# Optimization experiments

Measured on AMD Instinct MI355X. Metric: run time of the kernel, lower is better.

The kernel has to match this reference:

```python
import jax, jax.numpy as jnp
import numpy as np

N_NODES = 50000
N_EDGES = 600000
IN_F = 128
HID = 128
OUT = 128
CLS = 128
N_GRAPHS = 64
LN_EPS = 1e-5


def _ln(h, g, b):
    m = jnp.mean(h, axis=-1, keepdims=True)
    v = jnp.var(h, axis=-1, keepdims=True)
    return (h - m) * jax.lax.rsqrt(v + LN_EPS) * g + b


def _segment_softmax(logits, seg, num_segments):
    m = jax.ops.segment_max(logits, seg, num_segments=num_segments)
    e = jnp.exp(logits - m[seg])
    s = jax.ops.segment_sum(e, seg, num_segments=num_segments)
    return e / s[seg]


def _gat_conv(x, src, dst, aux, w_lin, b_lin, aw1, ab1, lng, lnb, aw2, ab2):
    xl = x @ w_lin + b_lin                      # [N, out]
    sf = xl[src]                                # [E, out]
    df = xl[dst]                                # [E, out]
    ef = jnp.concatenate([sf, df, aux], axis=-1)  # [E, 2*out+2]
    h = jax.nn.relu(_ln(ef @ aw1 + ab1, lng, lnb))
    logits = h @ aw2 + ab2                      # [E, 1]
    att = _segment_softmax(logits, dst, xl.shape[0])
    num = jax.ops.segment_sum(sf * att, dst, num_segments=xl.shape[0])
    cnt = jax.ops.segment_sum(jnp.ones((src.shape[0], 1), xl.dtype), dst, num_segments=xl.shape[0])
    out = num / jnp.maximum(cnt, 1.0)           # scatter_mean (empty rows -> 0)
    return out + xl


def setup_inputs() -> dict:
    key = jax.random.key(0)
    ks = jax.random.split(key, 24)
    s = 0.05
    d = {
        'x': jax.random.normal(ks[0], (N_NODES, IN_F), jnp.float32),
        'edge_index': jax.random.randint(ks[1], (2, N_EDGES), 0, N_NODES, jnp.int64),
        'aux_info': jax.random.normal(ks[2], (N_EDGES, 2), jnp.float32),
        'batch': jnp.sort(jax.random.randint(ks[3], (N_NODES,), 0, N_GRAPHS, jnp.int64)),
        # conv1 params (in->hid)
        'w_lin1': jax.random.normal(ks[4], (IN_F, HID), jnp.float32) * s,
        'b_lin1': jnp.zeros((HID,), jnp.float32),
        'aw1_1': jax.random.normal(ks[5], (2 * HID + 2, HID), jnp.float32) * s,
        'ab1_1': jnp.zeros((HID,), jnp.float32),
        'lng1': jnp.ones((HID,), jnp.float32),
        'lnb1': jnp.zeros((HID,), jnp.float32),
        'aw2_1': jax.random.normal(ks[6], (HID, 1), jnp.float32) * s,
        'ab2_1': jnp.zeros((1,), jnp.float32),
        # conv2 params (hid->out)
        'w_lin2': jax.random.normal(ks[7], (HID, OUT), jnp.float32) * s,
        'b_lin2': jnp.zeros((OUT,), jnp.float32),
        'aw1_2': jax.random.normal(ks[8], (2 * OUT + 2, HID), jnp.float32) * s,
        'ab1_2': jnp.zeros((HID,), jnp.float32),
        'lng2': jnp.ones((HID,), jnp.float32),
        'lnb2': jnp.zeros((HID,), jnp.float32),
        'aw2_2': jax.random.normal(ks[9], (HID, 1), jnp.float32) * s,
        'ab2_2': jnp.zeros((1,), jnp.float32),
        # head
        'cls_w': jax.random.normal(ks[10], (OUT, CLS), jnp.float32) * s,
        'cls_b': jnp.zeros((CLS,), jnp.float32),
        'norm_g': jnp.ones((OUT,), jnp.float32),
        'norm_b': jnp.zeros((OUT,), jnp.float32),
    }
    return d


def reference(x, edge_index, aux_info, batch,
              w_lin1, b_lin1, aw1_1, ab1_1, lng1, lnb1, aw2_1, ab2_1,
              w_lin2, b_lin2, aw1_2, ab1_2, lng2, lnb2, aw2_2, ab2_2,
              cls_w, cls_b, norm_g, norm_b):
    src, dst = edge_index[0], edge_index[1]
    h = _gat_conv(x, src, dst, aux_info, w_lin1, b_lin1, aw1_1, ab1_1, lng1, lnb1, aw2_1, ab2_1)
    h = jax.nn.relu(h)
    h = _gat_conv(h, src, dst, aux_info, w_lin2, b_lin2, aw1_2, ab1_2, lng2, lnb2, aw2_2, ab2_2)
    h = _ln(h, norm_g, norm_b)                  # [N, out]
    fusion = jax.ops.segment_max(h, batch, num_segments=N_GRAPHS)  # global max pool
    cls = fusion @ cls_w + cls_b                # [G, cls]
    return (h, cls)
```

## Files before the change

### kernel.cpp

```cpp
#include <hip/hip_runtime.h>
#include <math.h>

typedef __attribute__((ext_vector_type(8))) short short8v;
typedef __attribute__((ext_vector_type(4))) float f32x4;
typedef __attribute__((ext_vector_type(2))) float f32x2;

__device__ __forceinline__ unsigned short f2bf(float f) {
    union { float f; unsigned int u; } v; v.f = f;
    unsigned int r = v.u + 0x7FFFu + ((v.u >> 16) & 1u);
    return (unsigned short)(r >> 16);
}
__device__ __forceinline__ float bflo(unsigned int v) {
    union { unsigned int u; float f; } x; x.u = v << 16; return x.f;
}
__device__ __forceinline__ float bfhi(unsigned int v) {
    union { unsigned int u; float f; } x; x.u = v & 0xFFFF0000u; return x.f;
}
__device__ __forceinline__ unsigned char f2fp8(float f) {
    return (unsigned char)(__builtin_amdgcn_cvt_pk_fp8_f32(f, f, 0, false) & 0xFF);
}
__device__ __forceinline__ unsigned pkrtz(float a, float b) {
    unsigned d;
    asm("v_cvt_pkrtz_f16_f32 %0, %1, %2" : "=v"(d) : "v"(a), "v"(b));
    return d;
}
__device__ __forceinline__ float fdot2a(unsigned a, unsigned b, float c) {
    float d;
    asm("v_dot2_f32_f16 %0, %1, %2, %3" : "=v"(d) : "v"(a), "v"(b), "v"(c));
    return d;
}
__device__ __forceinline__ unsigned pk_fma_f16(unsigned a, unsigned b, unsigned c) {
    unsigned d;
    asm("v_pk_fma_f16 %0, %1, %2, %3" : "=v"(d) : "v"(a), "v"(b), "v"(c));
    return d;
}
__device__ __forceinline__ unsigned pk_max0_f16(unsigned a, unsigned z) {
    unsigned d;
    asm("v_pk_max_f16 %0, %1, %2" : "=v"(d) : "v"(a), "v"(z));
    return d;
}

__global__ __launch_bounds__(256) void prep_kernel(const float* __restrict__ s0,
                                                   const float* __restrict__ s1,
                                                   const float* __restrict__ s2,
                                                   const float* __restrict__ s3,
                                                   const float* __restrict__ s4,
                                                   const float* __restrict__ s5,
                                                   unsigned short* __restrict__ Wp,
                                                   const int* __restrict__ dst,
                                                   int* __restrict__ deg, int E) {
    int b = blockIdx.x;
    if (b < 384) {
        int which = b >> 6;
        const float* W = (which == 0) ? s0 : (which == 1) ? s1 : (which == 2) ? s2
                       : (which == 3) ? s3 : (which == 4) ? s4 : s5;
        int t = (b & 63) * 256 + threadIdx.x;
        int j = t & 7, l = (t >> 3) & 63, ct = (t >> 9) & 7, ks = t >> 12;
        int k = ks * 32 + (l >> 4) * 8 + j;
        int n = ct * 16 + (l & 15);
        Wp[which * 16384 + t] = f2bf(W[k * 128 + n]);
    } else {
        int e = (b - 384) * 256 + threadIdx.x;
        if (e < E) atomicAdd(&deg[dst[e]], 1);
    }
}

__global__ __launch_bounds__(256) void scan1_kernel(const int* __restrict__ deg,
                                                    int* __restrict__ rp,
                                                    int* __restrict__ bsum, int N) {
    const int lane = threadIdx.x & 63, wid = threadIdx.x >> 6;
    int i = blockIdx.x * 256 + threadIdx.x;
    int v = (i < N) ? deg[i] : 0;
    int val = v;
#pragma unroll
    for (int off = 1; off < 64; off <<= 1) {
        int t = __shfl_up(val, off, 64);
        if (lane >= off) val += t;
    }
    __shared__ int ws[4];
    if (lane == 63) ws[wid] = val;
    __syncthreads();
    int pre = 0;
#pragma unroll
    for (int w = 0; w < 4; ++w) pre += (w < wid) ? ws[w] : 0;
    int incl = pre + val;
    if (i < N) rp[i] = incl - v;
    if (threadIdx.x == 255) bsum[blockIdx.x] = incl;
}

__global__ __launch_bounds__(256) void scan23_kernel(int* __restrict__ rp,
                                                     const int* __restrict__ bsum,
                                                     const int* __restrict__ batch,
                                                     int* __restrict__ gstart,
                                                     int* __restrict__ gend,
                                                     int N, int E) {
    const int lane = threadIdx.x & 63, wid = threadIdx.x >> 6;
    const int b = blockIdx.x;
    int v = ((int)threadIdx.x < b) ? bsum[threadIdx.x] : 0;
#pragma unroll
    for (int m = 32; m >= 1; m >>= 1) v += __shfl_xor(v, m, 64);
    __shared__ int ws[4];
    if (lane == 0) ws[wid] = v;
    __syncthreads();
    int offset = ws[0] + ws[1] + ws[2] + ws[3];
    int i = b * 256 + threadIdx.x;
    if (i < N) {
        rp[i] += offset;
        int bb = batch[i];
        if (i == 0 || batch[i - 1] != bb) gstart[bb] = i;
        if (i == N - 1 || batch[i + 1] != bb) gend[bb] = i + 1;
    }
    if (b == 0 && threadIdx.x == 0) rp[N] = E;
}

__global__ void scatter_kernel(const int* __restrict__ src, const int* __restrict__ dst,
                               const float* __restrict__ aux,
                               const int* __restrict__ rowptr, int* __restrict__ cursor,
                               uint2* __restrict__ er, int E) {
    int e = blockIdx.x * 256 + threadIdx.x;
    if (e < E) {
        int d = dst[e];
        int pos = rowptr[d] + atomicAdd(&cursor[d], 1);
        float2 a = *(const float2*)(aux + 2 * e);
        uint2 r;
        r.x = (unsigned)src[e] | ((unsigned)d << 16);
        r.y = (unsigned)f2bf(a.x) | ((unsigned)f2bf(a.y) << 16);
        er[pos] = r;
    }
}

template <int ABF>
__global__ __launch_bounds__(256) void linpq_kernel(const void* __restrict__ Av,
                                                    const unsigned short* __restrict__ WpL,
                                                    const float* __restrict__ bias,
                                                    const unsigned short* __restrict__ WpP,
                                                    const unsigned short* __restrict__ WpQ,
                                                    const float* __restrict__ ab1,
                                                    unsigned short* __restrict__ Dbf,
                                                    unsigned char* __restrict__ Vf8,
                                                    unsigned char* __restrict__ Pf8,
                                                    unsigned char* __restrict__ Qf8, int M) {
    __shared__ unsigned short lds[32][136];
    __shared__ unsigned char ldsV[32][128];
    __shared__ unsigned char ldsP[32][128];
    __shared__ unsigned char ldsQ[32][128];
    const int l = threadIdx.x & 63, w = threadIdx.x >> 6;
    const int tile = w >> 1, ch = w & 1;
    const int rowb = blockIdx.x * 32;
    const int rowbase = rowb + tile * 16;
    const int r = rowbase + (l & 15);
    const int kc = (l >> 4) * 8;

    short8v afr[4];
    if (r < M) {
        if (ABF) {
            const unsigned short* ap = (const unsigned short*)Av + (size_t)r * 128 + kc;
#pragma unroll
            for (int ks = 0; ks < 4; ++ks)
                afr[ks] = *(const short8v*)(ap + ks * 32);
        } else {
            const float* ap = (const float*)Av + (size_t)r * 128 + kc;
#pragma unroll
            for (int ks = 0; ks < 4; ++ks) {
                float4 x0 = *(const float4*)(ap + ks * 32);
                float4 x1 = *(const float4*)(ap + ks * 32 + 4);
                unsigned short u[8] = {f2bf(x0.x), f2bf(x0.y), f2bf(x0.z), f2bf(x0.w),
                                       f2bf(x1.x), f2bf(x1.y), f2bf(x1.z), f2bf(x1.w)};
                afr[ks] = *(short8v*)u;
            }
        }
    } else {
#pragma unroll
        for (int ks = 0; ks < 4; ++ks)
#pragma unroll
            for (int j = 0; j < 8; ++j) afr[ks][j] = 0;
    }

    f32x4 acc[4];
#pragma unroll
    for (int c = 0; c < 4; ++c)
#pragma unroll
        for (int j = 0; j < 4; ++j) acc[c][j] = 0.f;

    const short8v* wl = (const short8v*)WpL;
#pragma unroll
    for (int ks = 0; ks < 4; ++ks)
#pragma unroll
        for (int c = 0; c < 4; ++c)
            acc[c] = __builtin_amdgcn_mfma_f32_16x16x32_bf16(
                afr[ks], wl[(ks * 8 + ch * 4 + c) * 64 + l], acc[c], 0, 0, 0);

    const int lrb = tile * 16 + (l >> 4) * 4;
#pragma unroll
    for (int c = 0; c < 4; ++c) {
        int col = (ch * 4 + c) * 16 + (l & 15);
        float bv = bias ? bias[col] : 0.f;
#pragma unroll
        for (int j = 0; j < 4; ++j) {
            float v = acc[c][j] + bv;
            lds[lrb + j][col] = f2bf(v);
            ldsV[lrb + j][col] = f2fp8(v);
        }
    }
    __syncthreads();

    {
        int r2 = threadIdx.x >> 3, q2 = threadIdx.x & 7;
        if (rowb + r2 < M) {
            *(uint4*)(Dbf + (size_t)(rowb + r2) * 128 + q2 * 16) =
                *(uint4*)&lds[r2][q2 * 16];
            *(uint4*)(Dbf + (size_t)(rowb + r2) * 128 + q2 * 16 + 8) =
                *(uint4*)&lds[r2][q2 * 16 + 8];
            *(uint4*)(Vf8 + (size_t)(rowb + r2) * 128 + q2 * 16) =
                *(uint4*)&ldsV[r2][q2 * 16];
        }
    }

    short8v xfr[4];
#pragma unroll
    for (int ks = 0; ks < 4; ++ks)
        xfr[ks] = *(const short8v*)&lds[tile * 16 + (l & 15)][kc + ks * 32];

    f32x4 accP[4], accQ[4];
#pragma unroll
    for (int c = 0; c < 4; ++c)
#pragma unroll
        for (int j = 0; j < 4; ++j) { accP[c][j] = 0.f; accQ[c][j] = 0.f; }

    const short8v* wp = (const short8v*)WpP;
    const short8v* wq = (const short8v*)WpQ;
#pragma unroll
    for (int ks = 0; ks < 4; ++ks)
#pragma unroll
        for (int c = 0; c < 4; ++c) {
            accP[c] = __builtin_amdgcn_mfma_f32_16x16x32_bf16(
                xfr[ks], wp[(ks * 8 + ch * 4 + c) * 64 + l], accP[c], 0, 0, 0);
            accQ[c] = __builtin_amdgcn_mfma_f32_16x16x32_bf16(
                xfr[ks], wq[(ks * 8 + ch * 4 + c) * 64 + l], accQ[c], 0, 0, 0);
        }

#pragma unroll
    for (int c = 0; c < 4; ++c) {
        int col = (ch * 4 + c) * 16 + (l & 15);
        float b1v = ab1[col];
#pragma unroll
        for (int j = 0; j < 4; ++j) {
            ldsP[lrb + j][col] = f2fp8(accP[c][j]);
            ldsQ[lrb + j][col] = f2fp8(accQ[c][j] + b1v);
        }
    }
    __syncthreads();
    {
        int r2 = threadIdx.x >> 3, q2 = threadIdx.x & 7;
        if (rowb + r2 < M) {
            *(uint4*)(Pf8 + (size_t)(rowb + r2) * 128 + q2 * 16) =
                *(uint4*)&ldsP[r2][q2 * 16];
            *(uint4*)(Qf8 + (size_t)(rowb + r2) * 128 + q2 * 16) =
                *(uint4*)&ldsQ[r2][q2 * 16];
        }
    }
}

__global__ __launch_bounds__(256, 4) void attn_edge_kernel(
    const unsigned char* __restrict__ Pf8, const unsigned char* __restrict__ Qf8,
    const uint2* __restrict__ er,
    const float* __restrict__ wa0, const float* __restrict__ wa1,
    const float* __restrict__ lng, const float* __restrict__ lnb,
    const float* __restrict__ aw2, const float* __restrict__ ab2,
    float* __restrict__ wt, int E) {
    __shared__ float lwf[256];
    __shared__ unsigned lwh[192];
    {
        int idx = threadIdx.x;
        int arr = idx >> 7, rem = idx & 127;
        int par = rem >> 6, c = (rem >> 2) & 15, e = rem & 3;
        const float* sp = arr ? wa1 : wa0;
        lwf[(((arr * 16 + c) << 1) + par) * 4 + e] = sp[rem];
        if (idx < 192) {
            int a2 = idx >> 6, rem2 = idx & 63;
            int p2 = rem2 >> 5;
            int c2 = (rem2 >> 1) & 15;
            int pr = rem2 & 1;
            int chn = p2 * 64 + c2 * 4 + pr * 2;
            const float* s2 = (a2 == 0) ? lng : (a2 == 1) ? lnb : aw2;
            lwh[(((a2 * 16 + c2) << 1) + p2) * 2 + pr] = pkrtz(s2[chn], s2[chn + 1]);
        }
    }
    __syncthreads();
    const int slot = blockIdx.x * 128 + ((int)threadIdx.x >> 1);
    if (slot >= E) return;
    const int par = threadIdx.x & 1;
    const unsigned one2 = 0x3C003C00u;
    const unsigned zero2 = 0u;
    const int co = par << 6;

    uint2 ev = er[slot];
    const int sn = (int)(ev.x & 0xFFFFu);
    const int dn = (int)(ev.x >> 16);
    const float ax = bflo(ev.y), ay = bfhi(ev.y);

    const uint4* prow = (const uint4*)(Pf8 + (size_t)sn * 128 + co);
    const uint4* qrow = (const uint4*)(Qf8 + (size_t)dn * 128 + co);

    float r1 = 0.f, r2 = 0.f;
    unsigned tp[32];

#pragma unroll
    for (int g = 0; g < 4; ++g) {
        uint4 pv = prow[g];
        uint4 qv = qrow[g];
        unsigned pwa[4] = {pv.x, pv.y, pv.z, pv.w};
        unsigned qwa[4] = {qv.x, qv.y, qv.z, qv.w};
#pragma unroll
        for (int cc = 0; cc < 4; ++cc) {
            const int c = g * 4 + cc;
            f32x2 plo = __builtin_amdgcn_cvt_pk_f32_fp8((int)pwa[cc], false);
            f32x2 phi = __builtin_amdgcn_cvt_pk_f32_fp8((int)pwa[cc], true);
            f32x2 qlo = __builtin_amdgcn_cvt_pk_f32_fp8((int)qwa[cc], false);
            f32x2 qhi = __builtin_amdgcn_cvt_pk_f32_fp8((int)qwa[cc], true);
            float4 w0v = *(const float4*)&lwf[((c << 1) + par) * 4];
            float4 w1v = *(const float4*)&lwf[(((16 + c) << 1) + par) * 4];
            float t0 = plo[0] + qlo[0] + ax * w0v.x + ay * w1v.x;
            float t1 = plo[1] + qlo[1] + ax * w0v.y + ay * w1v.y;
            float t2 = phi[0] + qhi[0] + ax * w0v.z + ay * w1v.z;
            float t3 = phi[1] + qhi[1] + ax * w0v.w + ay * w1v.w;
            unsigned p0 = pkrtz(t0, t1);
            unsigned p1 = pkrtz(t2, t3);
            tp[2 * c] = p0;
            tp[2 * c + 1] = p1;
            r1 = fdot2a(p0, one2, r1);
            r1 = fdot2a(p1, one2, r1);
            r2 = fdot2a(p0, p0, r2);
            r2 = fdot2a(p1, p1, r2);
        }
    }
    r1 += __shfl_xor(r1, 1, 64);
    r2 += __shfl_xor(r2, 1, 64);
    float mean = r1 * (1.f / 128.f);
    float rstd = rsqrtf(r2 * (1.f / 128.f) - mean * mean + 1e-5f);
    float mr = mean * rstd;
    unsigned rstd2 = pkrtz(rstd, rstd);
    unsigned nmr2 = pkrtz(-mr, -mr);

    float dot = 0.f;
#pragma unroll
    for (int c = 0; c < 16; ++c) {
        unsigned base = (unsigned)(((c << 1) + par) * 2);
        uint2 gg = *(const uint2*)&lwh[base];
        uint2 ll = *(const uint2*)&lwh[64 + base];
        uint2 ww = *(const uint2*)&lwh[128 + base];
        unsigned u0 = pk_fma_f16(tp[2 * c], rstd2, nmr2);
        u0 = pk_fma_f16(u0, gg.x, ll.x);
        u0 = pk_max0_f16(u0, zero2);
        dot = fdot2a(u0, ww.x, dot);
        unsigned u1 = pk_fma_f16(tp[2 * c + 1], rstd2, nmr2);
        u1 = pk_fma_f16(u1, gg.y, ll.y);
        u1 = pk_max0_f16(u1, zero2);
        dot = fdot2a(u1, ww.y, dot);
    }
    dot += __shfl_xor(dot, 1, 64);
    if (par == 0) wt[slot] = __expf(dot + ab2[0]);
}

template <int MODE>
__global__ __launch_bounds__(256) void aggr_kernel(
    const unsigned short* __restrict__ xlbf, const unsigned char* __restrict__ Vf8,
    const float* __restrict__ wt,
    const uint2* __restrict__ er, const int* __restrict__ rowptr,
    const float* __restrict__ g, const float* __restrict__ b,
    void* __restrict__ out, int N) {
    const int lane8 = threadIdx.x & 7;
    const int v = blockIdx.x * 32 + ((int)threadIdx.x >> 3);
    if (v >= N) return;
    const int jb = lane8 * 16;

    const int s0 = rowptr[v], s1e = rowptr[v + 1];
    const int deg = s1e - s0;
    float acc[16];
#pragma unroll
    for (int k = 0; k < 16; ++k) acc[k] = 0.f;
    float wsum = 0.f;

    uint4 v0 = make_uint4(0, 0, 0, 0), v1 = v0;
    float wb0 = 0.f, wb1 = 0.f;
#define GATH2(idx, VV, WW)                                                       \
    if ((idx) < s1e) {                                                           \
        int sn_ = (int)(er[idx].x & 0xFFFFu);                                    \
        VV = *(const uint4*)(Vf8 + (size_t)sn_ * 128 + jb);                      \
        WW = wt[idx];                                                            \
    }
    GATH2(s0, v0, wb0)
    GATH2(s0 + 1, v1, wb1)

    for (int i = s0; i < s1e; i += 2) {
        uint4 c0 = v0, c1 = v1;
        float u0 = wb0;
        float u1 = (i + 1 < s1e) ? wb1 : 0.f;
        GATH2(i + 2, v0, wb0)
        GATH2(i + 3, v1, wb1)
        wsum += u0 + u1;
        unsigned d0[4] = {c0.x, c0.y, c0.z, c0.w};
        unsigned d1[4] = {c1.x, c1.y, c1.z, c1.w};
#pragma unroll
        for (int k = 0; k < 4; ++k) {
            f32x2 alo = __builtin_amdgcn_cvt_pk_f32_fp8((int)d0[k], false);
            f32x2 ahi = __builtin_amdgcn_cvt_pk_f32_fp8((int)d0[k], true);
            f32x2 blo = __builtin_amdgcn_cvt_pk_f32_fp8((int)d1[k], false);
            f32x2 bhi = __builtin_amdgcn_cvt_pk_f32_fp8((int)d1[k], true);
            acc[4 * k + 0] += u0 * alo[0] + u1 * blo[0];
            acc[4 * k + 1] += u0 * alo[1] + u1 * blo[1];
            acc[4 * k + 2] += u0 * ahi[0] + u1 * bhi[0];
            acc[4 * k + 3] += u0 * ahi[1] + u1 * bhi[1];
        }
    }
#undef GATH2

    const float ns = (deg > 0) ? 1.f / (wsum * (float)deg) : 0.f;
    float o[16];
    const unsigned short* xp = xlbf + (size_t)v * 128 + jb;
    uint4 xa = *(const uint4*)xp;
    uint4 xb = *(const uint4*)(xp + 8);
    unsigned xw[8] = {xa.x, xa.y, xa.z, xa.w, xb.x, xb.y, xb.z, xb.w};
#pragma unroll
    for (int k = 0; k < 8; ++k) {
        o[2 * k] = bflo(xw[k]) + acc[2 * k] * ns;
        o[2 * k + 1] = bfhi(xw[k]) + acc[2 * k + 1] * ns;
    }

    if (MODE == 0) {
        unsigned short* op = (unsigned short*)out + (size_t)v * 128 + jb;
        unsigned opk[8];
#pragma unroll
        for (int k = 0; k < 8; ++k)
            opk[k] = (unsigned)f2bf(fmaxf(o[2 * k], 0.f)) |
                     ((unsigned)f2bf(fmaxf(o[2 * k + 1], 0.f)) << 16);
        *(uint4*)op = make_uint4(opk[0], opk[1], opk[2], opk[3]);
        *(uint4*)(op + 8) = make_uint4(opk[4], opk[5], opk[6], opk[7]);
    } else {
        float r1 = 0.f, r2 = 0.f;
#pragma unroll
        for (int k = 0; k < 16; ++k) { r1 += o[k]; r2 = fmaf(o[k], o[k], r2); }
#pragma unroll
        for (int mk = 4; mk >= 1; mk >>= 1) {
            r1 += __shfl_xor(r1, mk, 64);
            r2 += __shfl_xor(r2, mk, 64);
        }
        float mean = r1 * (1.f / 128.f);
        float rstd = rsqrtf(r2 * (1.f / 128.f) - mean * mean + 1e-5f);
        float mr = mean * rstd;
        float* op = (float*)out + (size_t)v * 128 + jb;
#pragma unroll
        for (int k4 = 0; k4 < 4; ++k4) {
            float4 gv = *(const float4*)(g + jb + 4 * k4);
            float4 bv = *(const float4*)(b + jb + 4 * k4);
            float4 r;
            r.x = fmaf(fmaf(o[4 * k4 + 0], rstd, -mr), gv.x, bv.x);
            r.y = fmaf(fmaf(o[4 * k4 + 1], rstd, -mr), gv.y, bv.y);
            r.z = fmaf(fmaf(o[4 * k4 + 2], rstd, -mr), gv.z, bv.z);
            r.w = fmaf(fmaf(o[4 * k4 + 3], rstd, -mr), gv.w, bv.w);
            *(float4*)(op + 4 * k4) = r;
        }
    }
}

__global__ __launch_bounds__(128) void pool1_kernel(const float* __restrict__ h,
                                                    const int* __restrict__ gstart,
                                                    const int* __restrict__ gend,
                                                    float* __restrict__ part) {
    int gph = blockIdx.x >> 4;
    int sl = blockIdx.x & 15;
    int col = threadIdx.x;
    int s = gstart[gph], e = gend[gph];
    float m = -INFINITY;
    for (int r = s + sl; r < e; r += 16) m = fmaxf(m, h[(size_t)r * 128 + col]);
    part[(size_t)blockIdx.x * 128 + col] = m;
}

__global__ __launch_bounds__(128) void cls_kernel(const float* __restrict__ part,
                                                  const float* __restrict__ cw,
                                                  const float* __restrict__ cb,
                                                  float* __restrict__ out) {
    int gph = blockIdx.x, c = threadIdx.x;
    float m = -INFINITY;
#pragma unroll
    for (int sl = 0; sl < 16; ++sl) m = fmaxf(m, part[(size_t)(gph * 16 + sl) * 128 + c]);
    __shared__ float f[128];
    f[c] = m;
    __syncthreads();
    float acc = cb[c];
#pragma unroll 8
    for (int k = 0; k < 128; ++k) acc += f[k] * cw[k * 128 + c];
    out[gph * 128 + c] = acc;
}

extern "C" void kernel_launch(void* const* d_in, const int* in_sizes, int n_in,
                              void* d_out, int out_size, void* d_ws, size_t ws_size,
                              hipStream_t stream) {
    const float* x      = (const float*)d_in[0];
    const int*   ei     = (const int*)d_in[1];
    const float* aux    = (const float*)d_in[2];
    const int*   batch  = (const int*)d_in[3];
    const float* w_lin1 = (const float*)d_in[4];
    const float* b_lin1 = (const float*)d_in[5];
    const float* aw1_1  = (const float*)d_in[6];
    const float* ab1_1  = (const float*)d_in[7];
    const float* lng1   = (const float*)d_in[8];
    const float* lnb1   = (const float*)d_in[9];
    const float* aw2_1  = (const float*)d_in[10];
    const float* ab2_1  = (const float*)d_in[11];
    const float* w_lin2 = (const float*)d_in[12];
    const float* b_lin2 = (const float*)d_in[13];
    const float* aw1_2  = (const float*)d_in[14];
    const float* ab1_2  = (const float*)d_in[15];
    const float* lng2   = (const float*)d_in[16];
    const float* lnb2   = (const float*)d_in[17];
    const float* aw2_2  = (const float*)d_in[18];
    const float* ab2_2  = (const float*)d_in[19];
    const float* cls_w  = (const float*)d_in[20];
    const float* cls_b  = (const float*)d_in[21];
    const float* norm_g = (const float*)d_in[22];
    const float* norm_b = (const float*)d_in[23];

    const int N = in_sizes[0] / 128;
    const int E = in_sizes[2] / 2;
    const int G = 64;
    const int* src = ei;
    const int* dst = ei + E;

    char* wsp = (char*)d_ws;
    unsigned short* xlbf  = (unsigned short*)wsp;   wsp += (size_t)N * 128 * 2;
    unsigned short* h1bf  = (unsigned short*)wsp;   wsp += (size_t)N * 128 * 2;
    unsigned char*  Pf8   = (unsigned char*)wsp;    wsp += (size_t)N * 128;
    unsigned char*  Qf8   = (unsigned char*)wsp;    wsp += (size_t)N * 128;
    unsigned char*  Vf8   = (unsigned char*)wsp;    wsp += (size_t)N * 128;
    unsigned short* wpack = (unsigned short*)wsp;   wsp += 6 * 16384 * 2;
    float*          part  = (float*)wsp;            wsp += (size_t)1024 * 128 * 4;
    uint2*          er    = (uint2*)wsp;            wsp += (size_t)E * 8;
    float*          wt    = (float*)wsp;            wsp += (size_t)E * 4;
    int*            bsum    = (int*)wsp;            wsp += 256 * 4;
    int*            deg     = (int*)wsp;            wsp += (size_t)N * 4;
    int*            cursor  = (int*)wsp;            wsp += (size_t)N * 4;
    int*            rowptr  = (int*)wsp;            wsp += (size_t)(N + 1) * 4;
    int*            gstart  = (int*)wsp;            wsp += (size_t)G * 4;
    int*            gend    = (int*)wsp;            wsp += (size_t)G * 4;

    unsigned short* wp_lin1 = wpack;
    unsigned short* wp_s1   = wpack + 16384;
    unsigned short* wp_d1   = wpack + 2 * 16384;
    unsigned short* wp_lin2 = wpack + 3 * 16384;
    unsigned short* wp_s2   = wpack + 4 * 16384;
    unsigned short* wp_d2   = wpack + 5 * 16384;

    float* hout   = (float*)d_out;
    float* clsout = hout + (size_t)N * 128;

    hipMemsetAsync(deg, 0, (size_t)(2 * N) * sizeof(int), stream);
    hipMemsetAsync(gstart, 0, (size_t)(2 * G) * sizeof(int), stream);

    const int eb = (E + 255) / 256;
    const int nb = (N + 255) / 256;
    const int lb = (N + 31) / 32;
    const int atb = (E + 127) / 128;
    const int agb = (N + 31) / 32;

    prep_kernel<<<384 + eb, 256, 0, stream>>>(w_lin1, aw1_1, aw1_1 + 128 * 128,
                                              w_lin2, aw1_2, aw1_2 + 128 * 128,
                                              wpack, dst, deg, E);
    scan1_kernel<<<nb, 256, 0, stream>>>(deg, rowptr, bsum, N);
    scan23_kernel<<<nb, 256, 0, stream>>>(rowptr, bsum, batch, gstart, gend, N, E);
    scatter_kernel<<<eb, 256, 0, stream>>>(src, dst, aux, rowptr, cursor, er, E);

    linpq_kernel<0><<<lb, 256, 0, stream>>>(x, wp_lin1, b_lin1, wp_s1, wp_d1, ab1_1,
                                            xlbf, Vf8, Pf8, Qf8, N);
    attn_edge_kernel<<<atb, 256, 0, stream>>>(Pf8, Qf8, er,
                                              aw1_1 + 256 * 128, aw1_1 + 257 * 128,
                                              lng1, lnb1, aw2_1, ab2_1, wt, E);
    aggr_kernel<0><<<agb, 256, 0, stream>>>(xlbf, Vf8, wt, er, rowptr,
                                            nullptr, nullptr, h1bf, N);
    linpq_kernel<1><<<lb, 256, 0, stream>>>(h1bf, wp_lin2, b_lin2, wp_s2, wp_d2, ab1_2,
                                            xlbf, Vf8, Pf8, Qf8, N);
    attn_edge_kernel<<<atb, 256, 0, stream>>>(Pf8, Qf8, er,
                                              aw1_2 + 256 * 128, aw1_2 + 257 * 128,
                                              lng2, lnb2, aw2_2, ab2_2, wt, E);
    aggr_kernel<1><<<agb, 256, 0, stream>>>(xlbf, Vf8, wt, er, rowptr,
                                            norm_g, norm_b, hout, N);
    pool1_kernel<<<G * 16, 128, 0, stream>>>(hout, gstart, gend, part);
    cls_kernel<<<G, 128, 0, stream>>>(part, cls_w, cls_b, clsout);
}
```

Measured before the change: 234.0 us.

## Precompute per-node LN mean sums, deepen aggr gather pipeline, nontemporal edge stores

The per-edge LayerNorm mean is now built by linearity from per-node row sums of the FP8 P and Q rows, which linpq writes out, plus the aux-weight sums reduced in shared memory. This removes the per-edge fdot2 accumulation of the first moment in the attention kernel. The aggregation kernel now prefetches four neighbour rows per iteration instead of two, for more memory-level parallelism, and the edge record becomes a 64-bit value written with a nontemporal store. The trade-offs are two extra N-sized arrays with extra scattered loads per edge, and the mean is computed in fp32 while the variance still uses fp16-rounded values, which may change numerics slightly.

```diff
diff --git a/kernel.cpp b/kernel.cpp
--- a/kernel.cpp
+++ b/kernel.cpp
@@ -116,16 +116,15 @@
 __global__ void scatter_kernel(const int* __restrict__ src, const int* __restrict__ dst,
                                const float* __restrict__ aux,
                                const int* __restrict__ rowptr, int* __restrict__ cursor,
-                               uint2* __restrict__ er, int E) {
+                               unsigned long long* __restrict__ er, int E) {
     int e = blockIdx.x * 256 + threadIdx.x;
     if (e < E) {
         int d = dst[e];
         int pos = rowptr[d] + atomicAdd(&cursor[d], 1);
         float2 a = *(const float2*)(aux + 2 * e);
-        uint2 r;
-        r.x = (unsigned)src[e] | ((unsigned)d << 16);
-        r.y = (unsigned)f2bf(a.x) | ((unsigned)f2bf(a.y) << 16);
-        er[pos] = r;
+        unsigned long long lo = (unsigned long long)((unsigned)src[e] | ((unsigned)d << 16));
+        unsigned long long hi = (unsigned long long)((unsigned)f2bf(a.x) | ((unsigned)f2bf(a.y) << 16));
+        __builtin_nontemporal_store(lo | (hi << 32), &er[pos]);
     }
 }
 
@@ -139,7 +138,9 @@
                                                     unsigned short* __restrict__ Dbf,
                                                     unsigned char* __restrict__ Vf8,
                                                     unsigned char* __restrict__ Pf8,
-                                                    unsigned char* __restrict__ Qf8, int M) {
+                                                    unsigned char* __restrict__ Qf8,
+                                                    float* __restrict__ sumP,
+                                                    float* __restrict__ sumQ, int M) {
     __shared__ unsigned short lds[32][136];
     __shared__ unsigned char ldsV[32][128];
     __shared__ unsigned char ldsP[32][128];
@@ -253,23 +254,46 @@
     {
         int r2 = threadIdx.x >> 3, q2 = threadIdx.x & 7;
         if (rowb + r2 < M) {
-            *(uint4*)(Pf8 + (size_t)(rowb + r2) * 128 + q2 * 16) =
-                *(uint4*)&ldsP[r2][q2 * 16];
-            *(uint4*)(Qf8 + (size_t)(rowb + r2) * 128 + q2 * 16) =
-                *(uint4*)&ldsQ[r2][q2 * 16];
+            uint4 pv = *(uint4*)&ldsP[r2][q2 * 16];
+            uint4 qv = *(uint4*)&ldsQ[r2][q2 * 16];
+            *(uint4*)(Pf8 + (size_t)(rowb + r2) * 128 + q2 * 16) = pv;
+            *(uint4*)(Qf8 + (size_t)(rowb + r2) * 128 + q2 * 16) = qv;
+            unsigned pw[4] = {pv.x, pv.y, pv.z, pv.w};
+            unsigned qw[4] = {qv.x, qv.y, qv.z, qv.w};
+            float sp = 0.f, sq = 0.f;
+#pragma unroll
+            for (int k = 0; k < 4; ++k) {
+                f32x2 a = __builtin_amdgcn_cvt_pk_f32_fp8((int)pw[k], false);
+                f32x2 b = __builtin_amdgcn_cvt_pk_f32_fp8((int)pw[k], true);
+                sp += (a[0] + a[1]) + (b[0] + b[1]);
+                f32x2 c = __builtin_amdgcn_cvt_pk_f32_fp8((int)qw[k], false);
+                f32x2 d = __builtin_amdgcn_cvt_pk_f32_fp8((int)qw[k], true);
+                sq += (c[0] + c[1]) + (d[0] + d[1]);
+            }
+#pragma unroll
+            for (int m = 4; m >= 1; m >>= 1) {
+                sp += __shfl_xor(sp, m, 64);
+                sq += __shfl_xor(sq, m, 64);
+            }
+            if (q2 == 0) {
+                sumP[rowb + r2] = sp;
+                sumQ[rowb + r2] = sq;
+            }
         }
     }
 }
 
 __global__ __launch_bounds__(256, 4) void attn_edge_kernel(
     const unsigned char* __restrict__ Pf8, const unsigned char* __restrict__ Qf8,
-    const uint2* __restrict__ er,
+    const float* __restrict__ sumP, const float* __restrict__ sumQ,
+    const unsigned long long* __restrict__ er,
     const float* __restrict__ wa0, const float* __restrict__ wa1,
     const float* __restrict__ lng, const float* __restrict__ lnb,
     const float* __restrict__ aw2, const float* __restrict__ ab2,
     float* __restrict__ wt, int E) {
     __shared__ float lwf[256];
     __shared__ unsigned lwh[192];
+    __shared__ float ssw[2];
     {
         int idx = threadIdx.x;
         int arr = idx >> 7, rem = idx & 127;
@@ -285,24 +309,35 @@
             const float* s2 = (a2 == 0) ? lng : (a2 == 1) ? lnb : aw2;
             lwh[(((a2 * 16 + c2) << 1) + p2) * 2 + pr] = pkrtz(s2[chn], s2[chn + 1]);
         }
+        int wv = idx >> 6, ln = idx & 63;
+        if (wv < 2) {
+            const float* s = wv ? wa1 : wa0;
+            float t = s[ln] + s[ln + 64];
+#pragma unroll
+            for (int m = 32; m >= 1; m >>= 1) t += __shfl_xor(t, m, 64);
+            if (ln == 0) ssw[wv] = t;
+        }
     }
     __syncthreads();
     const int slot = blockIdx.x * 128 + ((int)threadIdx.x >> 1);
     if (slot >= E) return;
     const int par = threadIdx.x & 1;
-    const unsigned one2 = 0x3C003C00u;
     const unsigned zero2 = 0u;
     const int co = par << 6;
-
-    uint2 ev = er[slot];
-    const int sn = (int)(ev.x & 0xFFFFu);
-    const int dn = (int)(ev.x >> 16);
-    const float ax = bflo(ev.y), ay = bfhi(ev.y);
+    const float sw0 = ssw[0], sw1 = ssw[1];
+
+    unsigned long long ev = er[slot];
+    const int sn = (int)(ev & 0xFFFFu);
+    const int dn = (int)((ev >> 16) & 0xFFFFu);
+    const unsigned ah = (unsigned)(ev >> 32);
+    const float ax = bflo(ah), ay = bfhi(ah);
+
+    const float mean = (sumP[sn] + sumQ[dn] + ax * sw0 + ay * sw1) * (1.f / 128.f);
 
     const uint4* prow = (const uint4*)(Pf8 + (size_t)sn * 128 + co);
     const uint4* qrow = (const uint4*)(Qf8 + (size_t)dn * 128 + co);
 
-    float r1 = 0.f, r2 = 0.f;
+    float r2 = 0.f;
     unsigned tp[32];
 
 #pragma unroll
@@ -328,15 +363,11 @@
             unsigned p1 = pkrtz(t2, t3);
             tp[2 * c] = p0;
             tp[2 * c + 1] = p1;
-            r1 = fdot2a(p0, one2, r1);
-            r1 = fdot2a(p1, one2, r1);
             r2 = fdot2a(p0, p0, r2);
             r2 = fdot2a(p1, p1, r2);
         }
     }
-    r1 += __shfl_xor(r1, 1, 64);
     r2 += __shfl_xor(r2, 1, 64);
-    float mean = r1 * (1.f / 128.f);
     float rstd = rsqrtf(r2 * (1.f / 128.f) - mean * mean + 1e-5f);
     float mr = mean * rstd;
     unsigned rstd2 = pkrtz(rstd, rstd);
@@ -366,7 +397,7 @@
 __global__ __launch_bounds__(256) void aggr_kernel(
     const unsigned short* __restrict__ xlbf, const unsigned char* __restrict__ Vf8,
     const float* __restrict__ wt,
-    const uint2* __restrict__ er, const int* __restrict__ rowptr,
+    const unsigned long long* __restrict__ er, const int* __restrict__ rowptr,
     const float* __restrict__ g, const float* __restrict__ b,
     void* __restrict__ out, int N) {
     const int lane8 = threadIdx.x & 7;
@@ -381,36 +412,50 @@
     for (int k = 0; k < 16; ++k) acc[k] = 0.f;
     float wsum = 0.f;
 
-    uint4 v0 = make_uint4(0, 0, 0, 0), v1 = v0;
-    float wb0 = 0.f, wb1 = 0.f;
+    uint4 pv[4];
+    float pw[4];
+#pragma unroll
+    for (int k = 0; k < 4; ++k) { pv[k] = make_uint4(0, 0, 0, 0); pw[k] = 0.f; }
 #define GATH2(idx, VV, WW)                                                       \
     if ((idx) < s1e) {                                                           \
-        int sn_ = (int)(er[idx].x & 0xFFFFu);                                    \
+        int sn_ = (int)(er[idx] & 0xFFFFu);                                      \
         VV = *(const uint4*)(Vf8 + (size_t)sn_ * 128 + jb);                      \
         WW = wt[idx];                                                            \
     }
-    GATH2(s0, v0, wb0)
-    GATH2(s0 + 1, v1, wb1)
-
-    for (int i = s0; i < s1e; i += 2) {
-        uint4 c0 = v0, c1 = v1;
-        float u0 = wb0;
-        float u1 = (i + 1 < s1e) ? wb1 : 0.f;
-        GATH2(i + 2, v0, wb0)
-        GATH2(i + 3, v1, wb1)
-        wsum += u0 + u1;
+    GATH2(s0 + 0, pv[0], pw[0])
+    GATH2(s0 + 1, pv[1], pw[1])
+    GATH2(s0 + 2, pv[2], pw[2])
+    GATH2(s0 + 3, pv[3], pw[3])
+
+    for (int i = s0; i < s1e; i += 4) {
+        uint4 c0 = pv[0], c1 = pv[1], c2 = pv[2], c3 = pv[3];
+        float u0 = pw[0];
+        float u1 = (i + 1 < s1e) ? pw[1] : 0.f;
+        float u2 = (i + 2 < s1e) ? pw[2] : 0.f;
+        float u3 = (i + 3 < s1e) ? pw[3] : 0.f;
+        GATH2(i + 4, pv[0], pw[0])
+        GATH2(i + 5, pv[1], pw[1])
+        GATH2(i + 6, pv[2], pw[2])
+        GATH2(i + 7, pv[3], pw[3])
+        wsum += (u0 + u1) + (u2 + u3);
         unsigned d0[4] = {c0.x, c0.y, c0.z, c0.w};
         unsigned d1[4] = {c1.x, c1.y, c1.z, c1.w};
+        unsigned d2[4] = {c2.x, c2.y, c2.z, c2.w};
+        unsigned d3[4] = {c3.x, c3.y, c3.z, c3.w};
 #pragma unroll
         for (int k = 0; k < 4; ++k) {
-            f32x2 alo = __builtin_amdgcn_cvt_pk_f32_fp8((int)d0[k], false);
-            f32x2 ahi = __builtin_amdgcn_cvt_pk_f32_fp8((int)d0[k], true);
-            f32x2 blo = __builtin_amdgcn_cvt_pk_f32_fp8((int)d1[k], false);
-            f32x2 bhi = __builtin_amdgcn_cvt_pk_f32_fp8((int)d1[k], true);
-            acc[4 * k + 0] += u0 * alo[0] + u1 * blo[0];
-            acc[4 * k + 1] += u0 * alo[1] + u1 * blo[1];
-            acc[4 * k + 2] += u0 * ahi[0] + u1 * bhi[0];
-            acc[4 * k + 3] += u0 * ahi[1] + u1 * bhi[1];
+            f32x2 a0 = __builtin_amdgcn_cvt_pk_f32_fp8((int)d0[k], false);
+            f32x2 a1 = __builtin_amdgcn_cvt_pk_f32_fp8((int)d0[k], true);
+            f32x2 b0 = __builtin_amdgcn_cvt_pk_f32_fp8((int)d1[k], false);
+            f32x2 b1 = __builtin_amdgcn_cvt_pk_f32_fp8((int)d1[k], true);
+            f32x2 e0 = __builtin_amdgcn_cvt_pk_f32_fp8((int)d2[k], false);
+            f32x2 e1 = __builtin_amdgcn_cvt_pk_f32_fp8((int)d2[k], true);
+            f32x2 f0 = __builtin_amdgcn_cvt_pk_f32_fp8((int)d3[k], false);
+            f32x2 f1 = __builtin_amdgcn_cvt_pk_f32_fp8((int)d3[k], true);
+            acc[4 * k + 0] += (u0 * a0[0] + u1 * b0[0]) + (u2 * e0[0] + u3 * f0[0]);
+            acc[4 * k + 1] += (u0 * a0[1] + u1 * b0[1]) + (u2 * e0[1] + u3 * f0[1]);
+            acc[4 * k + 2] += (u0 * a1[0] + u1 * b1[0]) + (u2 * e1[0] + u3 * f1[0]);
+            acc[4 * k + 3] += (u0 * a1[1] + u1 * b1[1]) + (u2 * e1[1] + u3 * f1[1]);
         }
     }
 #undef GATH2
@@ -535,8 +580,10 @@
     unsigned char*  Vf8   = (unsigned char*)wsp;    wsp += (size_t)N * 128;
     unsigned short* wpack = (unsigned short*)wsp;   wsp += 6 * 16384 * 2;
     float*          part  = (float*)wsp;            wsp += (size_t)1024 * 128 * 4;
-    uint2*          er    = (uint2*)wsp;            wsp += (size_t)E * 8;
+    unsigned long long* er = (unsigned long long*)wsp; wsp += (size_t)E * 8;
     float*          wt    = (float*)wsp;            wsp += (size_t)E * 4;
+    float*          sumP  = (float*)wsp;            wsp += (size_t)N * 4;
+    float*          sumQ  = (float*)wsp;            wsp += (size_t)N * 4;
     int*            bsum    = (int*)wsp;            wsp += 256 * 4;
     int*            deg     = (int*)wsp;            wsp += (size_t)N * 4;
     int*            cursor  = (int*)wsp;            wsp += (size_t)N * 4;
@@ -571,15 +618,15 @@
     scatter_kernel<<<eb, 256, 0, stream>>>(src, dst, aux, rowptr, cursor, er, E);
 
     linpq_kernel<0><<<lb, 256, 0, stream>>>(x, wp_lin1, b_lin1, wp_s1, wp_d1, ab1_1,
-                                            xlbf, Vf8, Pf8, Qf8, N);
-    attn_edge_kernel<<<atb, 256, 0, stream>>>(Pf8, Qf8, er,
+                                            xlbf, Vf8, Pf8, Qf8, sumP, sumQ, N);
+    attn_edge_kernel<<<atb, 256, 0, stream>>>(Pf8, Qf8, sumP, sumQ, er,
                                               aw1_1 + 256 * 128, aw1_1 + 257 * 128,
                                               lng1, lnb1, aw2_1, ab2_1, wt, E);
     aggr_kernel<0><<<agb, 256, 0, stream>>>(xlbf, Vf8, wt, er, rowptr,
                                             nullptr, nullptr, h1bf, N);
     linpq_kernel<1><<<lb, 256, 0, stream>>>(h1bf, wp_lin2, b_lin2, wp_s2, wp_d2, ab1_2,
-                                            xlbf, Vf8, Pf8, Qf8, N);
-    attn_edge_kernel<<<atb, 256, 0, stream>>>(Pf8, Qf8, er,
+                                            xlbf, Vf8, Pf8, Qf8, sumP, sumQ, N);
+    attn_edge_kernel<<<atb, 256, 0, stream>>>(Pf8, Qf8, sumP, sumQ, er,
                                               aw1_2 + 256 * 128, aw1_2 + 257 * 128,
                                               lng2, lnb2, aw2_2, ab2_2, wt, E);
     aggr_kernel<1><<<agb, 256, 0, stream>>>(xlbf, Vf8, wt, er, rowptr,
```

Result: slower. 255.7 us (+9.3%).
